# Performance work log

Hardware: AMD Instinct MI355X
Metric: run time of the kernel (lower is better)

Reference implementation:

```python
import jax, jax.numpy as jnp
import numpy as np

B, L, ENC, DEC, ATT = 128, 196, 2048, 512, 512

def setup_inputs() -> dict:
    key = jax.random.key(0)
    ks = jax.random.split(key, 8)
    s_enc = 1.0 / np.sqrt(ENC)
    s_dec = 1.0 / np.sqrt(DEC)
    s_att = 1.0 / np.sqrt(ATT)
    return {
        "encoder_out": jax.random.normal(ks[0], (B, L, ENC), jnp.float32),
        "decoder_hidden": jax.random.normal(ks[1], (B, DEC), jnp.float32),
        "We": jax.random.uniform(ks[2], (ENC, ATT), jnp.float32, -s_enc, s_enc),
        "be": jax.random.uniform(ks[3], (ATT,), jnp.float32, -s_enc, s_enc),
        "Wd": jax.random.uniform(ks[4], (DEC, ATT), jnp.float32, -s_dec, s_dec),
        "bd": jax.random.uniform(ks[5], (ATT,), jnp.float32, -s_dec, s_dec),
        "wa": jax.random.uniform(ks[6], (ATT,), jnp.float32, -s_att, s_att),
        "ba": jax.random.uniform(ks[7], (), jnp.float32, -s_att, s_att),
    }

def reference(encoder_out, decoder_hidden, We, be, Wd, bd, wa, ba):
    # encoder_out: [B, L, ENC]; decoder_hidden: [B, DEC]
    enc_map = jnp.einsum('ble,ea->bla', encoder_out, We) + be          # [B, L, A]
    dec_map = decoder_hidden @ Wd + bd                                  # [B, A]
    scores = jnp.tanh(enc_map + dec_map[:, None, :]) @ wa + ba         # [B, L]
    alphas = jax.nn.softmax(scores, axis=1)                             # [B, L]
    context = jnp.einsum('bl,ble->be', alphas, encoder_out)             # [B, ENC]
    return (context, alphas)
```

## Files before the change

kernel.cpp:

```cpp
#include <hip/hip_runtime.h>

#define B_   128
#define L_   196
#define ENC_ 2048
#define DEC_ 512
#define ATT_ 512
#define M_   (B_ * L_)

typedef _Float16 f16x8 __attribute__((ext_vector_type(8)));
typedef __fp16   h16x2 __attribute__((ext_vector_type(2)));
typedef float    f32x4 __attribute__((ext_vector_type(4)));

#define FENCE_LDS_BARRIER()                                        \
    do {                                                           \
        asm volatile("s_waitcnt lgkmcnt(0)" ::: "memory");         \
        __builtin_amdgcn_s_barrier();                              \
        __builtin_amdgcn_sched_barrier(0);                         \
    } while (0)


__global__ void wets_kernel(const float* __restrict__ We, _Float16* __restrict__ WeTs) {
    int u = blockIdx.x * 256 + threadIdx.x;
    int row = u & 127;
    int k8  = (u >> 7) & 3;
    int kt  = (u >> 9) & 63;
    int nt  = u >> 15;
    int n  = nt * 128 + row;
    int k0 = kt * 32 + k8 * 8;
    f16x8 h;
#pragma unroll
    for (int j = 0; j < 8; ++j) h[j] = (_Float16)We[(k0 + j) * ATT_ + n];
    *reinterpret_cast<f16x8*>(WeTs + (size_t)u * 8) = h;
}

__global__ void decmap_kernel(const float* __restrict__ dh, const float* __restrict__ Wd,
                              const float* __restrict__ bd, float* __restrict__ dec) {
    int b = blockIdx.x;
    int a = threadIdx.x;
    float acc = bd[a];
    const float* dhp = dh + b * DEC_;
#pragma unroll 8
    for (int k = 0; k < DEC_; ++k) acc += dhp[k] * Wd[k * ATT_ + a];
    dec[b * ATT_ + a] = acc;
}

__global__ __launch_bounds__(512) __attribute__((amdgpu_waves_per_eu(2, 2)))
void gemm_score_kernel(const float* __restrict__ enc,
                       const _Float16* __restrict__ WeTs,
                       const float* __restrict__ be,
                       const float* __restrict__ wa,
                       const float* __restrict__ dec,
                       float* __restrict__ scores) {
    __shared__ _Float16 As[2][4096];
    __shared__ float red[4][128];

    int mtile = blockIdx.x;
    int tid  = threadIdx.x;
    int lane = tid & 63, wid = tid >> 6;
    int wm = wid >> 2, wn = wid & 3;
    int l15 = lane & 15, lg = lane >> 4;

    int arowi = tid >> 2;
    int ac8   = tid & 3;
    const float* ag = enc + (size_t)(mtile * 128 + arowi) * ENC_ + ac8 * 8;
    int wa0 = (ac8 * 128 + (arowi ^ (2 * ac8))) * 8;

    const _Float16* bfr = WeTs +
        ((size_t)wn * 64 * 4 * 128 + (size_t)lg * 128 + l15) * 8;

    int afo = (lg * 128 + wm * 64 + (l15 ^ (2 * lg))) * 8;

    float4 areg0[2], areg1[2];
    f16x8  bf0[8], bf1[8];

    f32x4 acc[4][8];
#pragma unroll
    for (int mi = 0; mi < 4; ++mi)
#pragma unroll
        for (int ni = 0; ni < 8; ++ni) acc[mi][ni] = (f32x4){0.f, 0.f, 0.f, 0.f};

#define DEF_LOADA(S)                                                     \
    auto loadA##S = [&](int kt) {                                        \
        const float* a0 = ag + kt * 32;                                  \
        areg##S[0] = *reinterpret_cast<const float4*>(a0);               \
        areg##S[1] = *reinterpret_cast<const float4*>(a0 + 4);           \
    }
    DEF_LOADA(0); DEF_LOADA(1);
#undef DEF_LOADA

#define DEF_LOADB(S)                                                     \
    auto loadB##S = [&](int kt) {                                        \
        const _Float16* s = bfr + (size_t)kt * 4096;                     \
        bf##S[0] = *reinterpret_cast<const f16x8*>(s + 0 * 128);         \
        bf##S[1] = *reinterpret_cast<const f16x8*>(s + 1 * 128);         \
        bf##S[2] = *reinterpret_cast<const f16x8*>(s + 2 * 128);         \
        bf##S[3] = *reinterpret_cast<const f16x8*>(s + 3 * 128);         \
        bf##S[4] = *reinterpret_cast<const f16x8*>(s + 4 * 128);         \
        bf##S[5] = *reinterpret_cast<const f16x8*>(s + 5 * 128);         \
        bf##S[6] = *reinterpret_cast<const f16x8*>(s + 6 * 128);         \
        bf##S[7] = *reinterpret_cast<const f16x8*>(s + 7 * 128);         \
    }
    DEF_LOADB(0); DEF_LOADB(1);
#undef DEF_LOADB

#define DEF_WRITEA(S)                                                    \
    auto writeA##S = [&](int buf) {                                      \
        union { h16x2 h2[4]; f16x8 h8; } cv;                             \
        cv.h2[0] = __builtin_amdgcn_cvt_pkrtz(areg##S[0].x, areg##S[0].y); \
        cv.h2[1] = __builtin_amdgcn_cvt_pkrtz(areg##S[0].z, areg##S[0].w); \
        cv.h2[2] = __builtin_amdgcn_cvt_pkrtz(areg##S[1].x, areg##S[1].y); \
        cv.h2[3] = __builtin_amdgcn_cvt_pkrtz(areg##S[1].z, areg##S[1].w); \
        *reinterpret_cast<f16x8*>(&As[buf][wa0]) = cv.h8;                \
    }
    DEF_WRITEA(0); DEF_WRITEA(1);
#undef DEF_WRITEA

#define COMPUTE(BUF, BF)                                                 \
    do {                                                                 \
        f16x8 af[4];                                                     \
        _Pragma("unroll")                                                \
        for (int mi = 0; mi < 4; ++mi)                                   \
            af[mi] = *reinterpret_cast<const f16x8*>(&As[BUF][afo + mi * 128]); \
        __builtin_amdgcn_s_setprio(1);                                   \
        _Pragma("unroll")                                                \
        for (int mi = 0; mi < 4; ++mi)                                   \
            _Pragma("unroll")                                            \
            for (int ni = 0; ni < 8; ++ni)                               \
                acc[mi][ni] = __builtin_amdgcn_mfma_f32_16x16x32_f16(    \
                    af[mi], BF[ni], acc[mi][ni], 0, 0, 0);               \
        __builtin_amdgcn_s_setprio(0);                                   \
    } while (0)

    loadB0(0);
    __builtin_amdgcn_sched_barrier(0);
    loadA0(0);
    loadA1(1);
    writeA0(0);
    FENCE_LDS_BARRIER();

    for (int kt2 = 0; kt2 < 32; ++kt2) {
        int kt = kt2 * 2;
        loadB1(kt + 1);
        __builtin_amdgcn_sched_barrier(0);
        if (kt2 < 31) loadA0(kt + 2);
        COMPUTE(0, bf0);
        writeA1(1);
        FENCE_LDS_BARRIER();
        {
            int kb = kt + 2 < 64 ? kt + 2 : 63;
            loadB0(kb);
        }
        __builtin_amdgcn_sched_barrier(0);
        if (kt2 < 31) loadA1(kt + 3);
        COMPUTE(1, bf1);
        if (kt2 < 31) writeA0(0);
        FENCE_LDS_BARRIER();
    }
#undef COMPUTE

    float rsum[4][4];
#pragma unroll
    for (int mi = 0; mi < 4; ++mi)
#pragma unroll
        for (int j = 0; j < 4; ++j) rsum[mi][j] = 0.f;

    int rb = mtile * 128 + wm * 64;
#pragma unroll
    for (int ni = 0; ni < 8; ++ni) {
        int n = wn * 128 + ni * 16 + l15;
        float wav = wa[n];
        float bev = be[n];
#pragma unroll
        for (int mi = 0; mi < 4; ++mi) {
#pragma unroll
            for (int j = 0; j < 4; ++j) {
                int row = rb + mi * 16 + lg * 4 + j;
                int b = row / L_;
                float x = acc[mi][ni][j] + bev + dec[b * ATT_ + n];
                float e = __expf(2.0f * x);
                float t = 1.0f - 2.0f / (e + 1.0f);
                rsum[mi][j] += t * wav;
            }
        }
    }
#pragma unroll
    for (int mi = 0; mi < 4; ++mi) {
#pragma unroll
        for (int j = 0; j < 4; ++j) {
            float v = rsum[mi][j];
            v += __shfl_xor(v, 1);
            v += __shfl_xor(v, 2);
            v += __shfl_xor(v, 4);
            v += __shfl_xor(v, 8);
            if (l15 == 0) red[wn][wm * 64 + mi * 16 + lg * 4 + j] = v;
        }
    }
    __syncthreads();
    if (tid < 128)
        scores[mtile * 128 + tid] = red[0][tid] + red[1][tid] + red[2][tid] + red[3][tid];
}

__global__ void softmax_kernel(const float* __restrict__ scores, float* __restrict__ alphas) {
    int b = blockIdx.x, t = threadIdx.x;
    int lane = t & 63, wid = t >> 6;
    __shared__ float red[4];
    float s = 0.f, val = -1e30f;
    if (t < L_) {
        s = scores[b * L_ + t];
        val = s;
    }
    float m = val;
#pragma unroll
    for (int off = 1; off < 64; off <<= 1) m = fmaxf(m, __shfl_xor(m, off));
    if (lane == 0) red[wid] = m;
    __syncthreads();
    m = fmaxf(fmaxf(red[0], red[1]), fmaxf(red[2], red[3]));
    float e = (t < L_) ? __expf(s - m) : 0.f;
    float sum = e;
#pragma unroll
    for (int off = 1; off < 64; off <<= 1) sum += __shfl_xor(sum, off);
    __syncthreads();
    if (lane == 0) red[wid] = sum;
    __syncthreads();
    sum = red[0] + red[1] + red[2] + red[3];
    if (t < L_) alphas[b * L_ + t] = e / sum;
}

__global__ void context_kernel(const float* __restrict__ enc, const float* __restrict__ alphas,
                               float* __restrict__ ctx) {
    int b = blockIdx.x >> 2;
    int ec = blockIdx.x & 3;
    int e = ec * 512 + threadIdx.x * 2;
    const float* ep = enc + (size_t)b * L_ * ENC_ + e;
    const float* ap = alphas + b * L_;
    float ax = 0.f, ay = 0.f;
#pragma unroll 4
    for (int l = 0; l < L_; ++l) {
        float a = ap[l];
        float2 v = *reinterpret_cast<const float2*>(ep + (size_t)l * ENC_);
        ax += a * v.x;
        ay += a * v.y;
    }
    float2 r; r.x = ax; r.y = ay;
    *reinterpret_cast<float2*>(&ctx[b * ENC_ + e]) = r;
}

extern "C" void kernel_launch(void* const* d_in, const int* in_sizes, int n_in,
                              void* d_out, int out_size, void* d_ws, size_t ws_size,
                              hipStream_t stream) {
    const float* enc = (const float*)d_in[0];
    const float* dh  = (const float*)d_in[1];
    const float* We  = (const float*)d_in[2];
    const float* be  = (const float*)d_in[3];
    const float* Wd  = (const float*)d_in[4];
    const float* bd  = (const float*)d_in[5];
    const float* wa  = (const float*)d_in[6];

    float* out    = (float*)d_out;
    float* ctx    = out;
    float* alphas = out + B_ * ENC_;

    char* ws = (char*)d_ws;
    float*    dec     = (float*)ws;
    _Float16* WeTs    = (_Float16*)(ws + 262144);
    float*    scores  = (float*)(ws + 2359296);

    hipLaunchKernelGGL(wets_kernel,       dim3(512), dim3(256), 0, stream, We, WeTs);
    hipLaunchKernelGGL(decmap_kernel,     dim3(128), dim3(512), 0, stream, dh, Wd, bd, dec);
    hipLaunchKernelGGL(gemm_score_kernel, dim3(196), dim3(512), 0, stream, enc, WeTs, be, wa, dec, scores);
    hipLaunchKernelGGL(softmax_kernel,    dim3(128), dim3(256), 0, stream, scores, alphas);
    hipLaunchKernelGGL(context_kernel,    dim3(512), dim3(256), 0, stream, enc, alphas, ctx);
}
```

Measured before the change: 142.0 us.

## Split GEMM N across two blocks and stage B via LDS DMA triple buffering

Splits the fused score GEMM into two N-halves per M tile, giving 392 blocks of 256 threads instead of 196 blocks of 512. Each half writes a partial score that the softmax kernel sums. The B operand (We) now streams through a triple-buffered LDS ring using global_load_lds DMA instead of per-wave register loads, and the block-to-tile mapping is swizzled. The aim is better CU fill, since 196 blocks underfill the device, and less register pressure from B loads. The cost is that each A tile (encoder_out) is read and converted twice, raising global traffic, and the manual vmcnt waits add pipelining risk.

Result: no change. 141.2 us (-0.6%).

```diff
diff --git a/kernel.cpp b/kernel.cpp
--- a/kernel.cpp
+++ b/kernel.cpp
@@ -18,14 +18,20 @@
         __builtin_amdgcn_sched_barrier(0);                         \
     } while (0)
 
-
-__global__ void wets_kernel(const float* __restrict__ We, _Float16* __restrict__ WeTs) {
+__device__ __forceinline__ void gload16(const _Float16* g, _Float16* l) {
+    __builtin_amdgcn_global_load_lds(
+        (const __attribute__((address_space(1))) void*)g,
+        (__attribute__((address_space(3))) void*)l, 16, 0, 0);
+}
+
+
+__global__ void wets2_kernel(const float* __restrict__ We, _Float16* __restrict__ WeTs) {
     int u = blockIdx.x * 256 + threadIdx.x;
-    int row = u & 127;
-    int k8  = (u >> 7) & 3;
-    int kt  = (u >> 9) & 63;
-    int nt  = u >> 15;
-    int n  = nt * 128 + row;
+    int col = u & 255;
+    int k8  = (u >> 8) & 3;
+    int kt  = (u >> 10) & 63;
+    int nt  = u >> 16;
+    int n  = nt * 256 + col;
     int k0 = kt * 32 + k8 * 8;
     f16x8 h;
 #pragma unroll
@@ -44,7 +50,7 @@
     dec[b * ATT_ + a] = acc;
 }
 
-__global__ __launch_bounds__(512) __attribute__((amdgpu_waves_per_eu(2, 2)))
+__global__ __launch_bounds__(256, 2)
 void gemm_score_kernel(const float* __restrict__ enc,
                        const _Float16* __restrict__ WeTs,
                        const float* __restrict__ be,
@@ -52,26 +58,32 @@
                        const float* __restrict__ dec,
                        float* __restrict__ scores) {
     __shared__ _Float16 As[2][4096];
-    __shared__ float red[4][128];
-
-    int mtile = blockIdx.x;
+    __shared__ _Float16 Bs[3][8192];
+    __shared__ float red[2][128];
+
+    int bid = blockIdx.x;
+    int sid = (bid & 7) * 49 + (bid >> 3);
+    int mtile = sid >> 1;
+    int nt2   = sid & 1;
+
     int tid  = threadIdx.x;
     int lane = tid & 63, wid = tid >> 6;
-    int wm = wid >> 2, wn = wid & 3;
+    int wm = wid >> 1, wn = wid & 1;
     int l15 = lane & 15, lg = lane >> 4;
 
     int arowi = tid >> 2;
     int ac8   = tid & 3;
-    const float* ag = enc + (size_t)(mtile * 128 + arowi) * ENC_ + ac8 * 8;
+    const float* agA = enc + (size_t)(mtile * 128 + arowi) * ENC_ + ac8 * 8;
+    const float* agB = agA + (size_t)64 * ENC_;
     int wa0 = (ac8 * 128 + (arowi ^ (2 * ac8))) * 8;
-
-    const _Float16* bfr = WeTs +
-        ((size_t)wn * 64 * 4 * 128 + (size_t)lg * 128 + l15) * 8;
+    int wa1 = wa0 + 64 * 8;
+
+    const _Float16* bsrc = WeTs + ((size_t)nt2 * 64 * 1024 + tid) * 8;
 
     int afo = (lg * 128 + wm * 64 + (l15 ^ (2 * lg))) * 8;
-
-    float4 areg0[2], areg1[2];
-    f16x8  bf0[8], bf1[8];
+    int bfo = (lg * 256 + wn * 128 + l15) * 8;
+
+    float4 areg0[4], areg1[4];
 
     f32x4 acc[4][8];
 #pragma unroll
@@ -81,82 +93,101 @@
 
 #define DEF_LOADA(S)                                                     \
     auto loadA##S = [&](int kt) {                                        \
-        const float* a0 = ag + kt * 32;                                  \
+        const float* a0 = agA + kt * 32;                                 \
+        const float* a1 = agB + kt * 32;                                 \
         areg##S[0] = *reinterpret_cast<const float4*>(a0);               \
         areg##S[1] = *reinterpret_cast<const float4*>(a0 + 4);           \
+        areg##S[2] = *reinterpret_cast<const float4*>(a1);               \
+        areg##S[3] = *reinterpret_cast<const float4*>(a1 + 4);           \
     }
     DEF_LOADA(0); DEF_LOADA(1);
 #undef DEF_LOADA
 
-#define DEF_LOADB(S)                                                     \
-    auto loadB##S = [&](int kt) {                                        \
-        const _Float16* s = bfr + (size_t)kt * 4096;                     \
-        bf##S[0] = *reinterpret_cast<const f16x8*>(s + 0 * 128);         \
-        bf##S[1] = *reinterpret_cast<const f16x8*>(s + 1 * 128);         \
-        bf##S[2] = *reinterpret_cast<const f16x8*>(s + 2 * 128);         \
-        bf##S[3] = *reinterpret_cast<const f16x8*>(s + 3 * 128);         \
-        bf##S[4] = *reinterpret_cast<const f16x8*>(s + 4 * 128);         \
-        bf##S[5] = *reinterpret_cast<const f16x8*>(s + 5 * 128);         \
-        bf##S[6] = *reinterpret_cast<const f16x8*>(s + 6 * 128);         \
-        bf##S[7] = *reinterpret_cast<const f16x8*>(s + 7 * 128);         \
-    }
-    DEF_LOADB(0); DEF_LOADB(1);
-#undef DEF_LOADB
-
 #define DEF_WRITEA(S)                                                    \
     auto writeA##S = [&](int buf) {                                      \
+        _Float16* A_ = As[buf];                                          \
         union { h16x2 h2[4]; f16x8 h8; } cv;                             \
         cv.h2[0] = __builtin_amdgcn_cvt_pkrtz(areg##S[0].x, areg##S[0].y); \
         cv.h2[1] = __builtin_amdgcn_cvt_pkrtz(areg##S[0].z, areg##S[0].w); \
         cv.h2[2] = __builtin_amdgcn_cvt_pkrtz(areg##S[1].x, areg##S[1].y); \
         cv.h2[3] = __builtin_amdgcn_cvt_pkrtz(areg##S[1].z, areg##S[1].w); \
-        *reinterpret_cast<f16x8*>(&As[buf][wa0]) = cv.h8;                \
+        *reinterpret_cast<f16x8*>(A_ + wa0) = cv.h8;                     \
+        cv.h2[0] = __builtin_amdgcn_cvt_pkrtz(areg##S[2].x, areg##S[2].y); \
+        cv.h2[1] = __builtin_amdgcn_cvt_pkrtz(areg##S[2].z, areg##S[2].w); \
+        cv.h2[2] = __builtin_amdgcn_cvt_pkrtz(areg##S[3].x, areg##S[3].y); \
+        cv.h2[3] = __builtin_amdgcn_cvt_pkrtz(areg##S[3].z, areg##S[3].w); \
+        *reinterpret_cast<f16x8*>(A_ + wa1) = cv.h8;                     \
     }
     DEF_WRITEA(0); DEF_WRITEA(1);
 #undef DEF_WRITEA
 
-#define COMPUTE(BUF, BF)                                                 \
+#define DMAB(BUF, KT)                                                    \
     do {                                                                 \
-        f16x8 af[4];                                                     \
+        const _Float16* s_ = bsrc + (size_t)(KT) * 8192;                 \
+        gload16(s_,        &Bs[BUF][(0 * 256 + tid) * 8]);               \
+        gload16(s_ + 2048, &Bs[BUF][(1 * 256 + tid) * 8]);               \
+        gload16(s_ + 4096, &Bs[BUF][(2 * 256 + tid) * 8]);               \
+        gload16(s_ + 6144, &Bs[BUF][(3 * 256 + tid) * 8]);               \
+    } while (0)
+
+#define COMPUTE(RA, RB)                                                  \
+    do {                                                                 \
+        f16x8 af[4], bf[8];                                              \
         _Pragma("unroll")                                                \
         for (int mi = 0; mi < 4; ++mi)                                   \
-            af[mi] = *reinterpret_cast<const f16x8*>(&As[BUF][afo + mi * 128]); \
+            af[mi] = *reinterpret_cast<const f16x8*>(&As[RA][afo + mi * 128]); \
+        _Pragma("unroll")                                                \
+        for (int ni = 0; ni < 8; ++ni)                                   \
+            bf[ni] = *reinterpret_cast<const f16x8*>(&Bs[RB][bfo + ni * 128]); \
         __builtin_amdgcn_s_setprio(1);                                   \
         _Pragma("unroll")                                                \
         for (int mi = 0; mi < 4; ++mi)                                   \
             _Pragma("unroll")                                            \
             for (int ni = 0; ni < 8; ++ni)                               \
                 acc[mi][ni] = __builtin_amdgcn_mfma_f32_16x16x32_f16(    \
-                    af[mi], BF[ni], acc[mi][ni], 0, 0, 0);               \
+                    af[mi], bf[ni], acc[mi][ni], 0, 0, 0);               \
         __builtin_amdgcn_s_setprio(0);                                   \
     } while (0)
 
-    loadB0(0);
+#define PHASE(K, SA, RA, RB, DB, WS)                                     \
+    do {                                                                 \
+        int ka = (K) + 2 < 64 ? (K) + 2 : 63;                            \
+        loadA##SA(ka);                                                   \
+        __builtin_amdgcn_sched_barrier(0);                               \
+        COMPUTE(RA, RB);                                                 \
+        __builtin_amdgcn_sched_barrier(0);                               \
+        DMAB(DB, ka);                                                    \
+        __builtin_amdgcn_sched_barrier(0);                               \
+        writeA##WS(WS);                                                  \
+        asm volatile("s_waitcnt vmcnt(6)" ::: "memory");                 \
+        __builtin_amdgcn_sched_barrier(0);                               \
+        FENCE_LDS_BARRIER();                                             \
+    } while (0)
+
+    DMAB(0, 0);
+    DMAB(1, 1);
     __builtin_amdgcn_sched_barrier(0);
     loadA0(0);
     loadA1(1);
     writeA0(0);
     FENCE_LDS_BARRIER();
 
-    for (int kt2 = 0; kt2 < 32; ++kt2) {
-        int kt = kt2 * 2;
-        loadB1(kt + 1);
-        __builtin_amdgcn_sched_barrier(0);
-        if (kt2 < 31) loadA0(kt + 2);
-        COMPUTE(0, bf0);
-        writeA1(1);
-        FENCE_LDS_BARRIER();
-        {
-            int kb = kt + 2 < 64 ? kt + 2 : 63;
-            loadB0(kb);
-        }
-        __builtin_amdgcn_sched_barrier(0);
-        if (kt2 < 31) loadA1(kt + 3);
-        COMPUTE(1, bf1);
-        if (kt2 < 31) writeA0(0);
-        FENCE_LDS_BARRIER();
-    }
+    for (int k6 = 0; k6 < 10; ++k6) {
+        int k = k6 * 6;
+        PHASE(k + 0, 0, 0, 0, 2, 1);
+        PHASE(k + 1, 1, 1, 1, 0, 0);
+        PHASE(k + 2, 0, 0, 2, 1, 1);
+        PHASE(k + 3, 1, 1, 0, 2, 0);
+        PHASE(k + 4, 0, 0, 1, 0, 1);
+        PHASE(k + 5, 1, 1, 2, 1, 0);
+    }
+    PHASE(60, 0, 0, 0, 2, 1);
+    PHASE(61, 1, 1, 1, 0, 0);
+    PHASE(62, 0, 0, 2, 1, 1);
+    PHASE(63, 1, 1, 0, 2, 0);
+#undef PHASE
 #undef COMPUTE
+#undef DMAB
 
     float rsum[4][4];
 #pragma unroll
@@ -167,7 +198,7 @@
     int rb = mtile * 128 + wm * 64;
 #pragma unroll
     for (int ni = 0; ni < 8; ++ni) {
-        int n = wn * 128 + ni * 16 + l15;
+        int n = nt2 * 256 + wn * 128 + ni * 16 + l15;
         float wav = wa[n];
         float bev = be[n];
 #pragma unroll
@@ -196,8 +227,10 @@
         }
     }
     __syncthreads();
-    if (tid < 128)
-        scores[mtile * 128 + tid] = red[0][tid] + red[1][tid] + red[2][tid] + red[3][tid];
+    if (tid < 128) {
+        float v = red[0][tid] + red[1][tid];
+        scores[(size_t)nt2 * M_ + mtile * 128 + tid] = v;
+    }
 }
 
 __global__ void softmax_kernel(const float* __restrict__ scores, float* __restrict__ alphas) {
@@ -206,7 +239,8 @@
     __shared__ float red[4];
     float s = 0.f, val = -1e30f;
     if (t < L_) {
-        s = scores[b * L_ + t];
+        int r = b * L_ + t;
+        s = scores[r] + scores[M_ + r];
         val = s;
     }
     float m = val;
@@ -262,12 +296,12 @@
 
     char* ws = (char*)d_ws;
     float*    dec     = (float*)ws;
-    _Float16* WeTs    = (_Float16*)(ws + 262144);
+    _Float16* WeTs2   = (_Float16*)(ws + 262144);
     float*    scores  = (float*)(ws + 2359296);
 
-    hipLaunchKernelGGL(wets_kernel,       dim3(512), dim3(256), 0, stream, We, WeTs);
+    hipLaunchKernelGGL(wets2_kernel,      dim3(512), dim3(256), 0, stream, We, WeTs2);
     hipLaunchKernelGGL(decmap_kernel,     dim3(128), dim3(512), 0, stream, dh, Wd, bd, dec);
-    hipLaunchKernelGGL(gemm_score_kernel, dim3(196), dim3(512), 0, stream, enc, WeTs, be, wa, dec, scores);
+    hipLaunchKernelGGL(gemm_score_kernel, dim3(392), dim3(256), 0, stream, enc, WeTs2, be, wa, dec, scores);
     hipLaunchKernelGGL(softmax_kernel,    dim3(128), dim3(256), 0, stream, scores, alphas);
     hipLaunchKernelGGL(context_kernel,    dim3(512), dim3(256), 0, stream, enc, alphas, ctx);
 }
```
